# Kernel tuning notes

Measured on AMD Instinct MI355X. Metric: run time of the kernel, lower is better.

Reference implementation:

```python
import jax, jax.numpy as jnp
import numpy as np

S, R, CM, CZ, C, H = 128, 256, 256, 128, 32, 8
EPS = 1e-5


def layer_norm(x, w, b):
    mu = jnp.mean(x, axis=-1, keepdims=True)
    var = jnp.mean(jnp.square(x - mu), axis=-1, keepdims=True)
    return (x - mu) * jax.lax.rsqrt(var + EPS) * w + b


def setup_inputs() -> dict:
    key = jax.random.key(0)
    ks = jax.random.split(key, 10)
    s = 0.02
    return {
        "m": jax.random.normal(ks[0], (S, R, CM), jnp.float32),
        "z": jax.random.normal(ks[1], (R, R, CZ), jnp.float32),
        "ln_m_w": jnp.ones((CM,), jnp.float32),
        "ln_m_b": jnp.zeros((CM,), jnp.float32),
        "ln_z_w": jnp.ones((CZ,), jnp.float32),
        "ln_z_b": jnp.zeros((CZ,), jnp.float32),
        "Wz": jax.random.normal(ks[2], (CZ, H), jnp.float32) * s,
        "Wq": jax.random.normal(ks[3], (CM, H * C), jnp.float32) * s,
        "Wk": jax.random.normal(ks[4], (CM, H * C), jnp.float32) * s,
        "Wv": jax.random.normal(ks[5], (CM, H * C), jnp.float32) * s,
        "Wg": jax.random.normal(ks[6], (CM, H * C), jnp.float32) * s,
        "bg": jnp.ones((H * C,), jnp.float32),
        "Wo": jax.random.normal(ks[7], (H * C, CM), jnp.float32) * s,
        "bo": jnp.zeros((CM,), jnp.float32),
    }


def reference(m, z, ln_m_w, ln_m_b, ln_z_w, ln_z_b, Wz, Wq, Wk, Wv, Wg, bg, Wo, bo):
    mn = layer_norm(m, ln_m_w, ln_m_b)              # [S,R,CM]
    zn = layer_norm(z, ln_z_w, ln_z_b)              # [R,R,CZ]
    bias = jnp.einsum('qkz,zh->hqk', zn, Wz)        # [H,R,R] pair bias
    q = (mn @ Wq).reshape(S, R, H, C) * (C ** -0.5)
    k = (mn @ Wk).reshape(S, R, H, C)
    v = (mn @ Wv).reshape(S, R, H, C)
    logits = jnp.einsum('sqhc,skhc->shqk', q, k) + bias[None]  # [S,H,R,R]
    a = jax.nn.softmax(logits, axis=-1)
    o = jnp.einsum('shqk,skhc->sqhc', a, v)         # [S,R,H,C]
    g = jax.nn.sigmoid(mn @ Wg + bg).reshape(S, R, H, C)
    return (g * o).reshape(S, R, H * C) @ Wo + bo   # [S,R,CM]
```

## Files before the change

kernel.cpp:

```cpp
#include <hip/hip_runtime.h>
#include <math.h>

#define S_DIM 128
#define R_DIM 256
#define CM_DIM 256
#define CZ_DIM 128
#define C_DIM 32
#define H_DIM 8
#define HC_DIM 256
#define LN_EPS 1e-5f
#define ZPAD 132
#define HSZ 1048576
#define BIAS_SCALE 16384.0f
#define BIAS_INV (1.0f / 16384.0f)

typedef _Float16 half8 __attribute__((ext_vector_type(8)));
typedef _Float16 half4 __attribute__((ext_vector_type(4)));
typedef float f32x4 __attribute__((ext_vector_type(4)));
typedef short short4v __attribute__((ext_vector_type(4)));
typedef short short8v __attribute__((ext_vector_type(8)));

__device__ __forceinline__ float wave_sum(float v) {
#pragma unroll
    for (int off = 32; off > 0; off >>= 1) v += __shfl_down(v, off);
    return v;
}

__device__ __forceinline__ void gload16(const _Float16* src, _Float16* dst) {
    __builtin_amdgcn_global_load_lds((const __attribute__((address_space(1))) void*)src,
                                     (__attribute__((address_space(3))) void*)dst, 16, 0, 0);
}

__global__ __launch_bounds__(256) void convert_w_kernel(const float* __restrict__ Wq,
                                                        const float* __restrict__ Wk,
                                                        const float* __restrict__ Wv,
                                                        const float* __restrict__ Wg,
                                                        const float* __restrict__ Wo,
                                                        _Float16* __restrict__ w3) {
    int kb = blockIdx.x;
    int mat = blockIdx.y;
    const float* src = (mat == 0) ? Wq : (mat == 1) ? Wk : (mat == 2) ? Wv : (mat == 3) ? Wg : Wo;
    int n = threadIdx.x;
    _Float16 tmp[32];
#pragma unroll
    for (int kk = 0; kk < 32; kk++)
        tmp[kk] = (_Float16)src[(size_t)(kb * 32 + kk) * 256 + n];
    half8* dst = (half8*)(w3 + (size_t)mat * 65536 + (size_t)kb * 8192 + (size_t)n * 32);
#pragma unroll
    for (int i = 0; i < 4; i++) dst[i] = *(half8*)&tmp[i * 8];
}

__global__ __launch_bounds__(64) void prep_wz_kernel(const float* __restrict__ w,
                                                     const float* __restrict__ b,
                                                     const float* __restrict__ Wz,
                                                     float* __restrict__ u_g,
                                                     float* __restrict__ UB) {
    int lane = threadIdx.x;
    float w0 = w[lane], w1 = w[lane + 64];
    float b0 = b[lane], b1 = b[lane + 64];
#pragma unroll
    for (int h = 0; h < H_DIM; h++) {
        float wz0 = Wz[lane * H_DIM + h], wz1 = Wz[(lane + 64) * H_DIM + h];
        float u0 = w0 * wz0, u1 = w1 * wz1;
        u_g[h * ZPAD + lane] = u0;
        u_g[h * ZPAD + lane + 64] = u1;
        float U = wave_sum(u0 + u1);
        float B = wave_sum(b0 * wz0 + b1 * wz1);
        if (lane == 0) { UB[h] = U; UB[8 + h] = B; }
    }
}

__global__ __launch_bounds__(64) void ln_m_kernel(const float* __restrict__ m,
                                                  const float* __restrict__ w,
                                                  const float* __restrict__ b,
                                                  _Float16* __restrict__ mn) {
    int row = blockIdx.x;
    int t = threadIdx.x;
    const float4* mrow = (const float4*)(m + (size_t)row * CM_DIM);
    float4 x = mrow[t];
    float s = x.x + x.y + x.z + x.w;
    float ss = x.x * x.x + x.y * x.y + x.z * x.z + x.w * x.w;
    s = wave_sum(s);
    ss = wave_sum(ss);
    s = __shfl(s, 0);
    ss = __shfl(ss, 0);
    float mean = s * (1.0f / CM_DIM);
    float var = ss * (1.0f / CM_DIM) - mean * mean;
    float rsig = rsqrtf(var + LN_EPS);
    float4 wv = ((const float4*)w)[t];
    float4 bv = ((const float4*)b)[t];
    half4 o;
    o[0] = (_Float16)((x.x - mean) * rsig * wv.x + bv.x);
    o[1] = (_Float16)((x.y - mean) * rsig * wv.y + bv.y);
    o[2] = (_Float16)((x.z - mean) * rsig * wv.z + bv.z);
    o[3] = (_Float16)((x.w - mean) * rsig * wv.w + bv.w);
    *(half4*)(mn + (size_t)row * CM_DIM + t * 4) = o;
}

__global__ __launch_bounds__(256) void ln_z_bias_kernel(const float* __restrict__ z,
                                                        const float* __restrict__ u_g,
                                                        const float* __restrict__ UB,
                                                        short* __restrict__ bias_i) {
    __shared__ __align__(16) float zt[64 * ZPAD];
    __shared__ __align__(16) float ut[8 * ZPAD];
    __shared__ float UBs[16];
    int tid = threadIdx.x;
    int row0 = blockIdx.x * 64;
    for (int i = tid; i < 8 * ZPAD; i += 256) ut[i] = u_g[i];
    if (tid < 16) UBs[tid] = UB[tid];
    const float4* zsrc = (const float4*)(z + (size_t)row0 * CZ_DIM);
#pragma unroll
    for (int i = 0; i < 8; i++) {
        int idx = tid + i * 256;
        float4 v = zsrc[idx];
        int r = idx >> 5, c4 = (idx & 31) * 4;
        *(float4*)&zt[r * ZPAD + c4] = v;
    }
    __syncthreads();
    int r = tid >> 2, p = tid & 3;
    const float* zr = &zt[r * ZPAD];
    const float* u0p = &ut[p * ZPAD];
    const float* u1p = &ut[(p + 4) * ZPAD];
    float s = 0.f, ss = 0.f, a0 = 0.f, a1 = 0.f;
#pragma unroll
    for (int c = 0; c < CZ_DIM; c += 4) {
        float4 x = *(const float4*)&zr[c];
        float4 uu0 = *(const float4*)&u0p[c];
        float4 uu1 = *(const float4*)&u1p[c];
        s += x.x + x.y + x.z + x.w;
        ss += x.x * x.x + x.y * x.y + x.z * x.z + x.w * x.w;
        a0 += x.x * uu0.x + x.y * uu0.y + x.z * uu0.z + x.w * uu0.w;
        a1 += x.x * uu1.x + x.y * uu1.y + x.z * uu1.z + x.w * uu1.w;
    }
    float mu = s * (1.0f / CZ_DIM);
    float var = ss * (1.0f / CZ_DIM) - mu * mu;
    float rsig = rsqrtf(var + LN_EPS);
    int row = row0 + r;
    float b0v = rsig * (a0 - mu * UBs[p]) + UBs[8 + p];
    float b1v = rsig * (a1 - mu * UBs[4 + p]) + UBs[12 + p];
    int i0 = (int)rintf(b0v * BIAS_SCALE);
    int i1 = (int)rintf(b1v * BIAS_SCALE);
    i0 = i0 > 32767 ? 32767 : (i0 < -32768 ? -32768 : i0);
    i1 = i1 > 32767 ? 32767 : (i1 < -32768 ? -32768 : i1);
    bias_i[(size_t)p * 65536 + row] = (short)i0;
    bias_i[(size_t)(p + 4) * 65536 + row] = (short)i1;
}

__global__ __launch_bounds__(256, 3) void proj_mfma_kernel(const _Float16* __restrict__ A,
                                                           const _Float16* __restrict__ w3,
                                                           const float* __restrict__ bg,
                                                           _Float16* __restrict__ qh,
                                                           _Float16* __restrict__ kh,
                                                           _Float16* __restrict__ vh,
                                                           _Float16* __restrict__ gh) {
    __shared__ _Float16 Bs[2][64 * 128];
    __shared__ _Float16 Os[64 * 132];
    int m0 = blockIdx.x * 64;
    int col0 = blockIdx.y * 128;
    int tid = threadIdx.x, lane = tid & 63, wave = tid >> 6;
    int lrow = lane & 15, g = lane >> 4;
    int wr = wave >> 1, wc = wave & 1;
    const float qscale = 0.17677669529663687f;

    half8 afr[2][8];
#pragma unroll
    for (int mf = 0; mf < 2; mf++)
#pragma unroll
        for (int kb = 0; kb < 8; kb++)
            afr[mf][kb] = *(const half8*)(A + (size_t)(m0 + wr * 32 + mf * 16 + lrow) * 256 +
                                          kb * 32 + g * 8);

#define STAGE_B(T, BUF)                                                              \
    {                                                                                \
        int mat_ = (T) >> 2, kp_ = (T) & 3;                                          \
        _Float16* dst_ = &Bs[BUF][0];                                                \
        const _Float16* src_ = w3 + (size_t)mat_ * 65536 + (size_t)kp_ * 16384;      \
        _Pragma("unroll") for (int i_ = 0; i_ < 4; i_++) {                           \
            int j_ = tid + i_ * 256;                                                 \
            int n_ = j_ >> 3, cL_ = j_ & 7;                                          \
            int c_ = cL_ ^ (n_ & 7);                                                 \
            int kbL_ = c_ >> 2, q_ = c_ & 3;                                         \
            gload16(src_ + (size_t)kbL_ * 8192 + (size_t)(col0 + n_) * 32 + q_ * 8,  \
                    dst_ + (size_t)j_ * 8);                                          \
        }                                                                            \
    }

    STAGE_B(0, 0);
    STAGE_B(1, 1);
    __syncthreads();

    f32x4 acc[2][4];
    for (int t = 0; t < 16; t++) {
        int buf = t & 1;
        int mat = t >> 2, kp = t & 3;
        if (kp == 0) {
#pragma unroll
            for (int i = 0; i < 2; i++)
#pragma unroll
                for (int j = 0; j < 4; j++) acc[i][j] = (f32x4){0.f, 0.f, 0.f, 0.f};
        }
#pragma unroll
        for (int kbL = 0; kbL < 2; kbL++) {
            int kb = kp * 2 + kbL;
            half8 bf[4];
#pragma unroll
            for (int nf = 0; nf < 4; nf++) {
                int col = wc * 64 + nf * 16 + lrow;
                int chunk = (kbL * 4 + g) ^ (col & 7);
                bf[nf] = *(half8*)&Bs[buf][(size_t)(col * 8 + chunk) * 8];
            }
#pragma unroll
            for (int mf = 0; mf < 2; mf++)
#pragma unroll
                for (int nf = 0; nf < 4; nf++)
                    acc[mf][nf] = __builtin_amdgcn_mfma_f32_16x16x32_f16(afr[mf][kb], bf[nf],
                                                                         acc[mf][nf], 0, 0, 0);
        }
        if (kp == 3) {
#pragma unroll
            for (int mf = 0; mf < 2; mf++)
#pragma unroll
                for (int nf = 0; nf < 4; nf++)
#pragma unroll
                    for (int ri = 0; ri < 4; ri++) {
                        int srow = wr * 32 + mf * 16 + g * 4 + ri;
                        int scol = wc * 64 + nf * 16 + lrow;
                        float v = acc[mf][nf][ri];
                        if (mat == 0) v *= qscale;
                        if (mat == 3) v = 1.0f / (1.0f + __expf(-(v + bg[col0 + scol])));
                        Os[srow * 132 + scol] = (_Float16)v;
                    }
            __syncthreads();
            if (mat < 3) {
                _Float16* Out = (mat == 0) ? qh : (mat == 1) ? kh : vh;
#pragma unroll
                for (int j = 0; j < 4; j++) {
                    int hh = (col0 >> 5) + j;
                    int row = tid >> 2, cOff = (tid & 3) * 8;
                    half8 v8 = *(half8*)&Os[row * 132 + j * 32 + cOff];
                    *(half8*)(Out + (size_t)hh * HSZ + (size_t)(m0 + row) * 32 + cOff) = v8;
                }
            } else {
#pragma unroll
                for (int i = 0; i < 4; i++) {
                    int c2 = tid + i * 256;
                    int row = c2 >> 4, cOff = (c2 & 15) * 8;
                    half8 v8 = *(half8*)&Os[row * 132 + cOff];
                    *(half8*)(gh + (size_t)(m0 + row) * 256 + col0 + cOff) = v8;
                }
            }
        }
        __syncthreads();
        if (t + 2 < 16) STAGE_B(t + 2, buf);
    }
#undef STAGE_B
}

__global__ __launch_bounds__(1024, 1) void attn_mfma_kernel(const _Float16* __restrict__ qh,
                                                            const _Float16* __restrict__ kh,
                                                            const _Float16* __restrict__ vh,
                                                            const _Float16* __restrict__ gh,
                                                            const short* __restrict__ bias_i,
                                                            _Float16* __restrict__ oh) {
    __shared__ short bias_s[256][264];
    __shared__ _Float16 K_s[2][64][40];
    __shared__ _Float16 VT_s[2][32][68];
    int h = blockIdx.x, sg = blockIdx.y;
    int tid = threadIdx.x;
    int grp = tid >> 9;
    int t5 = tid & 511;
    int lane = tid & 63, wave = t5 >> 6;
    int lrow = lane & 15, g = lane >> 4, lk8 = g * 8;
    int qw = wave * 32;

    const short* bsrc = bias_i + (size_t)h * 65536;
#pragma unroll
    for (int i = 0; i < 8; i++) {
        int e = (tid + i * 1024) * 8;
        short8v v = *(const short8v*)(bsrc + e);
        *(short8v*)&bias_s[e >> 8][e & 255] = v;
    }

    const _Float16* qbase = qh + (size_t)h * HSZ;
    const _Float16* kbase = kh + (size_t)h * HSZ;
    const _Float16* vbase = vh + (size_t)h * HSZ;
    _Float16* obase = oh + (size_t)h * HSZ;

    bool isK = (wave < 4);
    int key = (t5 & 255) >> 2, koff = (t5 & 3) * 8;
    int vkey = t5 & 63, vc0 = ((t5 >> 6) & 3) * 8;

    for (int si = 0; si < 2; si++) {
        int s = sg * 4 + grp * 2 + si;
        half8 qfr[2];
#pragma unroll
        for (int qf = 0; qf < 2; qf++)
            qfr[qf] = *(const half8*)(qbase + (size_t)(s * 256 + qw + qf * 16 + lrow) * 32 + lk8);

        f32x4 oaccT[2][2];
        float m_run[2], l_run[2];
#pragma unroll
        for (int qf = 0; qf < 2; qf++) {
            oaccT[qf][0] = (f32x4){0.f, 0.f, 0.f, 0.f};
            oaccT[qf][1] = (f32x4){0.f, 0.f, 0.f, 0.f};
            m_run[qf] = -1e30f;
            l_run[qf] = 0.f;
        }

        half8 stg;
        if (isK) stg = *(const half8*)(kbase + (size_t)(s * 256 + key) * 32 + koff);
        else     stg = *(const half8*)(vbase + (size_t)(s * 256 + vkey) * 32 + vc0);

        for (int kb = 0; kb < 4; kb++) {
            __syncthreads();
            if (isK) {
                *(half8*)&K_s[grp][key][koff] = stg;
            } else {
#pragma unroll
                for (int j = 0; j < 8; j++) VT_s[grp][vc0 + j][vkey] = stg[j];
            }
            if (kb < 3) {
                int nk = (kb + 1) * 64;
                if (isK) stg = *(const half8*)(kbase + (size_t)(s * 256 + nk + key) * 32 + koff);
                else     stg = *(const half8*)(vbase + (size_t)(s * 256 + nk + vkey) * 32 + vc0);
            }
            __syncthreads();

            half8 kfr[4];
#pragma unroll
            for (int kf = 0; kf < 4; kf++) kfr[kf] = *(half8*)&K_s[grp][kf * 16 + lrow][lk8];

#pragma unroll
            for (int qf = 0; qf < 2; qf++) {
                f32x4 sf[4];
#pragma unroll
                for (int kf = 0; kf < 4; kf++) {
                    f32x4 zero = (f32x4){0.f, 0.f, 0.f, 0.f};
                    sf[kf] = __builtin_amdgcn_mfma_f32_16x16x32_f16(kfr[kf], qfr[qf], zero, 0, 0, 0);
                }
                int q = qw + qf * 16 + lrow;
#pragma unroll
                for (int kf = 0; kf < 4; kf++) {
                    short4v bh = *(short4v*)&bias_s[q][kb * 64 + kf * 16 + 4 * g];
#pragma unroll
                    for (int ri = 0; ri < 4; ri++) sf[kf][ri] += (float)bh[ri] * BIAS_INV;
                }
                float tm = -1e30f;
#pragma unroll
                for (int kf = 0; kf < 4; kf++)
#pragma unroll
                    for (int ri = 0; ri < 4; ri++) tm = fmaxf(tm, sf[kf][ri]);
                tm = fmaxf(tm, __shfl_xor(tm, 16));
                tm = fmaxf(tm, __shfl_xor(tm, 32));
                float nm = fmaxf(m_run[qf], tm);
                float sc = __expf(m_run[qf] - nm);
                m_run[qf] = nm;
                oaccT[qf][0] *= sc;
                oaccT[qf][1] *= sc;
                float rs = 0.f;
                half4 pfr[4];
#pragma unroll
                for (int kf = 0; kf < 4; kf++)
#pragma unroll
                    for (int ri = 0; ri < 4; ri++) {
                        float pv = __expf(sf[kf][ri] - nm);
                        rs += pv;
                        pfr[kf][ri] = (_Float16)pv;
                    }
                rs += __shfl_xor(rs, 16);
                rs += __shfl_xor(rs, 32);
                l_run[qf] = l_run[qf] * sc + rs;
#pragma unroll
                for (int kf = 0; kf < 4; kf++)
#pragma unroll
                    for (int cf = 0; cf < 2; cf++) {
                        half4 va = *(half4*)&VT_s[grp][cf * 16 + lrow][kf * 16 + 4 * g];
                        oaccT[qf][cf] = __builtin_amdgcn_mfma_f32_16x16x16f16(va, pfr[kf],
                                                                              oaccT[qf][cf], 0, 0, 0);
                    }
            }
        }
#pragma unroll
        for (int qf = 0; qf < 2; qf++) {
            float inv = 1.0f / l_run[qf];
            int q = qw + qf * 16 + lrow;
#pragma unroll
            for (int cf = 0; cf < 2; cf++) {
                half4 gv4 = *(const half4*)(gh + (size_t)(s * 256 + q) * 256 + h * 32 + cf * 16 + 4 * g);
                half4 o4;
#pragma unroll
                for (int ri = 0; ri < 4; ri++)
                    o4[ri] = (_Float16)(oaccT[qf][cf][ri] * inv * (float)gv4[ri]);
                *(half4*)(obase + (size_t)(s * 256 + q) * 32 + cf * 16 + 4 * g) = o4;
            }
        }
    }
}

__global__ __launch_bounds__(256, 4) void out_mfma_kernel(const _Float16* __restrict__ oh,
                                                          const _Float16* __restrict__ w3o,
                                                          const float* __restrict__ bo,
                                                          float* __restrict__ out) {
    __shared__ _Float16 Bs[2][64 * 128];
    int m0 = blockIdx.x * 64;
    int col0 = blockIdx.y * 128;
    int tid = threadIdx.x, lane = tid & 63, wave = tid >> 6;
    int lrow = lane & 15, g = lane >> 4;
    int wr = wave >> 1, wc = wave & 1;

    half8 afr[2][8];
#pragma unroll
    for (int mf = 0; mf < 2; mf++)
#pragma unroll
        for (int kb = 0; kb < 8; kb++)
            afr[mf][kb] = *(const half8*)(oh + (size_t)kb * HSZ +
                                          (size_t)(m0 + wr * 32 + mf * 16 + lrow) * 32 + g * 8);

#define STAGE_BO(T, BUF)                                                             \
    {                                                                                \
        int kp_ = (T);                                                               \
        _Float16* dst_ = &Bs[BUF][0];                                                \
        const _Float16* src_ = w3o + (size_t)kp_ * 16384;                            \
        _Pragma("unroll") for (int i_ = 0; i_ < 4; i_++) {                           \
            int j_ = tid + i_ * 256;                                                 \
            int n_ = j_ >> 3, cL_ = j_ & 7;                                          \
            int c_ = cL_ ^ (n_ & 7);                                                 \
            int kbL_ = c_ >> 2, q_ = c_ & 3;                                         \
            gload16(src_ + (size_t)kbL_ * 8192 + (size_t)(col0 + n_) * 32 + q_ * 8,  \
                    dst_ + (size_t)j_ * 8);                                          \
        }                                                                            \
    }

    STAGE_BO(0, 0);
    STAGE_BO(1, 1);
    __syncthreads();

    f32x4 acc[2][4];
#pragma unroll
    for (int i = 0; i < 2; i++)
#pragma unroll
        for (int j = 0; j < 4; j++) acc[i][j] = (f32x4){0.f, 0.f, 0.f, 0.f};

    for (int t = 0; t < 4; t++) {
        int buf = t & 1;
#pragma unroll
        for (int kbL = 0; kbL < 2; kbL++) {
            int kb = t * 2 + kbL;
            half8 bf[4];
#pragma unroll
            for (int nf = 0; nf < 4; nf++) {
                int col = wc * 64 + nf * 16 + lrow;
                int chunk = (kbL * 4 + g) ^ (col & 7);
                bf[nf] = *(half8*)&Bs[buf][(size_t)(col * 8 + chunk) * 8];
            }
#pragma unroll
            for (int mf = 0; mf < 2; mf++)
#pragma unroll
                for (int nf = 0; nf < 4; nf++)
                    acc[mf][nf] = __builtin_amdgcn_mfma_f32_16x16x32_f16(afr[mf][kb], bf[nf],
                                                                         acc[mf][nf], 0, 0, 0);
        }
        __syncthreads();
        if (t + 2 < 4) STAGE_BO(t + 2, buf);
    }
#undef STAGE_BO

#pragma unroll
    for (int mf = 0; mf < 2; mf++)
#pragma unroll
        for (int nf = 0; nf < 4; nf++)
#pragma unroll
            for (int ri = 0; ri < 4; ri++) {
                int row = m0 + wr * 32 + mf * 16 + g * 4 + ri;
                int col = col0 + wc * 64 + nf * 16 + lrow;
                out[(size_t)row * 256 + col] = acc[mf][nf][ri] + bo[col];
            }
}

extern "C" void kernel_launch(void* const* d_in, const int* in_sizes, int n_in,
                              void* d_out, int out_size, void* d_ws, size_t ws_size,
                              hipStream_t stream) {
    const float* m = (const float*)d_in[0];
    const float* z = (const float*)d_in[1];
    const float* ln_m_w = (const float*)d_in[2];
    const float* ln_m_b = (const float*)d_in[3];
    const float* ln_z_w = (const float*)d_in[4];
    const float* ln_z_b = (const float*)d_in[5];
    const float* Wz = (const float*)d_in[6];
    const float* Wq = (const float*)d_in[7];
    const float* Wk = (const float*)d_in[8];
    const float* Wv = (const float*)d_in[9];
    const float* Wg = (const float*)d_in[10];
    const float* bg = (const float*)d_in[11];
    const float* Wo = (const float*)d_in[12];
    const float* bo = (const float*)d_in[13];
    float* out = (float*)d_out;

    const size_t NE = (size_t)S_DIM * R_DIM * CM_DIM;
    _Float16* hb = (_Float16*)d_ws;
    _Float16* mn_h = hb;
    _Float16* qh = hb + NE;
    _Float16* kh = hb + 2 * NE;
    _Float16* vh = hb + 3 * NE;
    _Float16* gh = hb + 4 * NE;
    _Float16* oh = hb + 5 * NE;
    _Float16* w3 = hb + 6 * NE;
    float* u_g = (float*)(hb + 6 * NE + 5 * 65536);
    float* UB = u_g + 8 * ZPAD;
    short* bias_i = (short*)(UB + 16);

    hipLaunchKernelGGL(convert_w_kernel, dim3(8, 5), dim3(256), 0, stream,
                       Wq, Wk, Wv, Wg, Wo, w3);
    hipLaunchKernelGGL(prep_wz_kernel, dim3(1), dim3(64), 0, stream,
                       ln_z_w, ln_z_b, Wz, u_g, UB);
    hipLaunchKernelGGL(ln_m_kernel, dim3(S_DIM * R_DIM), dim3(64), 0, stream,
                       m, ln_m_w, ln_m_b, mn_h);
    hipLaunchKernelGGL(ln_z_bias_kernel, dim3(1024), dim3(256), 0, stream,
                       z, u_g, UB, bias_i);
    hipLaunchKernelGGL(proj_mfma_kernel, dim3(512, 2), dim3(256), 0, stream,
                       mn_h, w3, bg, qh, kh, vh, gh);
    hipLaunchKernelGGL(attn_mfma_kernel, dim3(H_DIM, 32), dim3(1024), 0, stream,
                       qh, kh, vh, gh, bias_i, oh);
    hipLaunchKernelGGL(out_mfma_kernel, dim3(512, 2), dim3(256), 0, stream,
                       oh, w3 + 4 * 65536, bo, out);
}
```

Before: 116.2 us.

## Stage projection A tile in LDS and split epilogue into two half-width passes

```diff
diff --git a/kernel.cpp b/kernel.cpp
--- a/kernel.cpp
+++ b/kernel.cpp
@@ -146,15 +146,16 @@
     bias_i[(size_t)(p + 4) * 65536 + row] = (short)i1;
 }
 
-__global__ __launch_bounds__(256, 3) void proj_mfma_kernel(const _Float16* __restrict__ A,
+__global__ __launch_bounds__(256, 2) void proj_mfma_kernel(const _Float16* __restrict__ A,
                                                            const _Float16* __restrict__ w3,
                                                            const float* __restrict__ bg,
                                                            _Float16* __restrict__ qh,
                                                            _Float16* __restrict__ kh,
                                                            _Float16* __restrict__ vh,
                                                            _Float16* __restrict__ gh) {
+    __shared__ _Float16 As[64 * 256];
     __shared__ _Float16 Bs[2][64 * 128];
-    __shared__ _Float16 Os[64 * 132];
+    __shared__ _Float16 Os[64 * 66];
     int m0 = blockIdx.x * 64;
     int col0 = blockIdx.y * 128;
     int tid = threadIdx.x, lane = tid & 63, wave = tid >> 6;
@@ -162,13 +163,13 @@
     int wr = wave >> 1, wc = wave & 1;
     const float qscale = 0.17677669529663687f;
 
-    half8 afr[2][8];
-#pragma unroll
-    for (int mf = 0; mf < 2; mf++)
-#pragma unroll
-        for (int kb = 0; kb < 8; kb++)
-            afr[mf][kb] = *(const half8*)(A + (size_t)(m0 + wr * 32 + mf * 16 + lrow) * 256 +
-                                          kb * 32 + g * 8);
+#pragma unroll
+    for (int i = 0; i < 8; i++) {
+        int j = tid + i * 256;
+        int row = j >> 5;
+        int c = (j & 31) ^ (row & 7);
+        gload16(A + (size_t)(m0 + row) * 256 + c * 8, As + (size_t)j * 8);
+    }
 
 #define STAGE_B(T, BUF)                                                              \
     {                                                                                \
@@ -202,7 +203,12 @@
 #pragma unroll
         for (int kbL = 0; kbL < 2; kbL++) {
             int kb = kp * 2 + kbL;
-            half8 bf[4];
+            half8 af[2], bf[4];
+#pragma unroll
+            for (int mf = 0; mf < 2; mf++) {
+                int row = wr * 32 + mf * 16 + lrow;
+                af[mf] = *(half8*)&As[row * 256 + (((kb * 4 + g) ^ (row & 7)) * 8)];
+            }
 #pragma unroll
             for (int nf = 0; nf < 4; nf++) {
                 int col = wc * 64 + nf * 16 + lrow;
@@ -213,40 +219,49 @@
             for (int mf = 0; mf < 2; mf++)
 #pragma unroll
                 for (int nf = 0; nf < 4; nf++)
-                    acc[mf][nf] = __builtin_amdgcn_mfma_f32_16x16x32_f16(afr[mf][kb], bf[nf],
+                    acc[mf][nf] = __builtin_amdgcn_mfma_f32_16x16x32_f16(af[mf], bf[nf],
                                                                          acc[mf][nf], 0, 0, 0);
         }
         if (kp == 3) {
 #pragma unroll
-            for (int mf = 0; mf < 2; mf++)
-#pragma unroll
-                for (int nf = 0; nf < 4; nf++)
-#pragma unroll
-                    for (int ri = 0; ri < 4; ri++) {
-                        int srow = wr * 32 + mf * 16 + g * 4 + ri;
-                        int scol = wc * 64 + nf * 16 + lrow;
-                        float v = acc[mf][nf][ri];
-                        if (mat == 0) v *= qscale;
-                        if (mat == 3) v = 1.0f / (1.0f + __expf(-(v + bg[col0 + scol])));
-                        Os[srow * 132 + scol] = (_Float16)v;
+            for (int hf2 = 0; hf2 < 2; hf2++) {
+                __syncthreads();
+                if (wc == hf2) {
+#pragma unroll
+                    for (int mf = 0; mf < 2; mf++)
+#pragma unroll
+                        for (int nf = 0; nf < 4; nf++)
+#pragma unroll
+                            for (int ri = 0; ri < 4; ri++) {
+                                int srow = wr * 32 + mf * 16 + g * 4 + ri;
+                                int scol = nf * 16 + lrow;
+                                float v = acc[mf][nf][ri];
+                                if (mat == 0) v *= qscale;
+                                if (mat == 3)
+                                    v = 1.0f / (1.0f + __expf(-(v + bg[col0 + hf2 * 64 + scol])));
+                                Os[srow * 66 + scol] = (_Float16)v;
+                            }
+                }
+                __syncthreads();
+                if (mat < 3) {
+                    _Float16* Out = (mat == 0) ? qh : (mat == 1) ? kh : vh;
+#pragma unroll
+                    for (int i = 0; i < 2; i++) {
+                        int j = tid + i * 256;
+                        int slab = j >> 8, jj = j & 255;
+                        int row = jj >> 2, cOff = (jj & 3) * 8;
+                        half8 v8 = *(half8*)&Os[row * 66 + slab * 32 + cOff];
+                        *(half8*)(Out + (size_t)((col0 >> 5) + hf2 * 2 + slab) * HSZ +
+                                  (size_t)(m0 + row) * 32 + cOff) = v8;
                     }
-            __syncthreads();
-            if (mat < 3) {
-                _Float16* Out = (mat == 0) ? qh : (mat == 1) ? kh : vh;
-#pragma unroll
-                for (int j = 0; j < 4; j++) {
-                    int hh = (col0 >> 5) + j;
-                    int row = tid >> 2, cOff = (tid & 3) * 8;
-                    half8 v8 = *(half8*)&Os[row * 132 + j * 32 + cOff];
-                    *(half8*)(Out + (size_t)hh * HSZ + (size_t)(m0 + row) * 32 + cOff) = v8;
-                }
-            } else {
-#pragma unroll
-                for (int i = 0; i < 4; i++) {
-                    int c2 = tid + i * 256;
-                    int row = c2 >> 4, cOff = (c2 & 15) * 8;
-                    half8 v8 = *(half8*)&Os[row * 132 + cOff];
-                    *(half8*)(gh + (size_t)(m0 + row) * 256 + col0 + cOff) = v8;
+                } else {
+#pragma unroll
+                    for (int i = 0; i < 2; i++) {
+                        int j = tid + i * 256;
+                        int row = j >> 3, cOff = (j & 7) * 8;
+                        half8 v8 = *(half8*)&Os[row * 66 + cOff];
+                        *(half8*)(gh + (size_t)(m0 + row) * 256 + col0 + hf2 * 64 + cOff) = v8;
+                    }
                 }
             }
         }
```

Result: slower. 121.0 us (+4.1%).
